# Performance work log

Hardware: AMD Instinct MI355X
Metric: run time of the kernel (lower is better)

Reference implementation:

```python
import jax, jax.numpy as jnp
import numpy as np

N = 100000   # nodes in batch
E = 1600000  # edges
H = 128      # hidden_channels
G = 500      # number of subgraphs (batch ids)
MAXZ = 1000  # max_z
L = 3        # num_layers


def setup_inputs() -> dict:
    key = jax.random.key(0)
    ks = jax.random.split(key, 12)
    s = 1.0 / np.sqrt(H)
    z = jax.random.randint(ks[0], (N,), 0, MAXZ)
    edge_index = jax.random.randint(ks[1], (2, E), 0, N)
    batch = jnp.repeat(jnp.arange(G), N // G)  # sorted graph ids, 200 nodes/graph
    edge_weight = jax.random.uniform(ks[2], (E,), jnp.float32)
    z_table = jax.random.normal(ks[3], (MAXZ, H), jnp.float32) * s
    conv_Ws = tuple(jax.random.normal(ks[4 + i], (H, H), jnp.float32) * s for i in range(L))
    conv_bs = tuple(jnp.zeros((H,), jnp.float32) for _ in range(L))
    lin1_W = jax.random.normal(ks[8], (H, H), jnp.float32) * s
    lin1_b = jnp.zeros((H,), jnp.float32)
    lin2_W = jax.random.normal(ks[9], (H, 1), jnp.float32) * s
    lin2_b = jnp.zeros((1,), jnp.float32)
    return dict(z=z, edge_index=edge_index, batch=batch, edge_weight=edge_weight,
                z_table=z_table, conv_Ws=conv_Ws, conv_bs=conv_bs,
                lin1_W=lin1_W, lin1_b=lin1_b, lin2_W=lin2_W, lin2_b=lin2_b)


def gcn_norm(edge_index, edge_weight, n):
    # add self loops (fill value 1) and symmetric normalization, as in PyG gcn_norm
    loop = jnp.arange(n)
    row = jnp.concatenate([edge_index[0], loop])
    col = jnp.concatenate([edge_index[1], loop])
    w = jnp.concatenate([edge_weight, jnp.ones((n,), edge_weight.dtype)])
    deg = jax.ops.segment_sum(w, col, num_segments=n)
    dinv = jnp.where(deg > 0, jax.lax.rsqrt(deg), 0.0)
    norm = dinv[row] * w * dinv[col]
    return row, col, norm


def gcn_conv(x, row, col, norm, W, b):
    xw = x @ W                                        # [N,H] GEMM first (PyG order)
    msg = norm[:, None] * xw[row]                     # gather + scale  [E+N, H]
    out = jax.ops.segment_sum(msg, col, num_segments=x.shape[0])  # scatter-add
    return out + b


def reference(z, edge_index, batch, edge_weight, z_table, conv_Ws, conv_bs,
              lin1_W, lin1_b, lin2_W, lin2_b):
    x = z_table[z]                                    # z embedding [N,H]
    row, col, norm = gcn_norm(edge_index, edge_weight, x.shape[0])
    for i in range(L - 1):
        x = jax.nn.relu(gcn_conv(x, row, col, norm, conv_Ws[i], conv_bs[i]))
        # dropout is identity in eval mode
    x = gcn_conv(x, row, col, norm, conv_Ws[-1], conv_bs[-1])
    # first occurrence of each graph id in sorted batch == center node indices
    center = jnp.searchsorted(batch, jnp.arange(G))
    h = x[center] * x[center + 1]                     # src * dst center pair
    h = jax.nn.relu(h @ lin1_W + lin1_b)
    return h @ lin2_W + lin2_b                        # [G,1]
```

## Files before the change

### kernel.cpp

```cpp
#include <hip/hip_runtime.h>
#include <hip/hip_bf16.h>

#define H 128
#define CAP 64
#define GBM 64
#define GBN 64
#define BW 128
#define BSH 7
#define BCAP 4096
#define EPB 2048
#define RSHIFT 17
#define RMASK  0x1FFFF

typedef __attribute__((ext_vector_type(8))) short bf16x8;
typedef __attribute__((ext_vector_type(4))) float f32x4;
typedef unsigned long long u64;

__device__ __forceinline__ unsigned short f2b(float f) {
  __hip_bfloat16 h = __float2bfloat16(f);
  union { __hip_bfloat16 h; unsigned short u; } c; c.h = h; return c.u;
}
__device__ __forceinline__ float b2f(unsigned short u) {
  union { unsigned int i; float f; } c; c.i = (unsigned)u << 16; return c.f;
}


__global__ __launch_bounds__(256) void k_binA(const int* __restrict__ row,
    const int* __restrict__ col, const float* __restrict__ ew,
    int* __restrict__ gcur, u64* __restrict__ binned, int E, int NB) {
  __shared__ int hist[1024];
  __shared__ int gbase[1024];
  int tid = threadIdx.x;
  for (int i = tid; i < NB; i += 256) hist[i] = 0;
  __syncthreads();
  int base = blockIdx.x * EPB;
  for (int j = tid; j < EPB; j += 256) {
    int e = base + j;
    if (e < E) atomicAdd(&hist[col[e] >> BSH], 1);
  }
  __syncthreads();
  for (int i = tid; i < NB; i += 256) {
    gbase[i] = atomicAdd(&gcur[i], hist[i]);
    hist[i] = 0;
  }
  __syncthreads();
  for (int j = tid; j < EPB; j += 256) {
    int e = base + j;
    if (e < E) {
      int c = col[e];
      int b = c >> BSH;
      int r = atomicAdd(&hist[b], 1);
      int pos = gbase[b] + r;
      if (pos >= BCAP) pos = BCAP - 1;
      unsigned pk = (unsigned)(c & (BW - 1)) | ((unsigned)row[e] << BSH);
      binned[(size_t)b * BCAP + pos] = (u64)pk | ((u64)(unsigned)__float_as_int(ew[e]) << 32);
    }
  }
}


__global__ __launch_bounds__(256) void k_binB(const int* __restrict__ gcur,
    const u64* __restrict__ binned, int* __restrict__ cnt, float* __restrict__ dinv,
    int2* __restrict__ elist, int n) {
  __shared__ int lcnt[BW];
  __shared__ float lws[BW];
  __shared__ int lcur[BW];
  int b = blockIdx.x, tid = threadIdx.x;
  if (tid < BW) { lcnt[tid] = 0; lws[tid] = 0.f; lcur[tid] = 0; }
  __syncthreads();
  int m = gcur[b];
  if (m > BCAP) m = BCAP;
  const u64* src = binned + (size_t)b * BCAP;
  for (int j = tid; j < m; j += 256) {
    u64 v = src[j];
    int cl = (int)(v & (BW - 1));
    atomicAdd(&lcnt[cl], 1);
    atomicAdd(&lws[cl], __int_as_float((int)(v >> 32)));
  }
  __syncthreads();
  if (tid < BW) {
    int c = b * BW + tid;
    if (c < n) {
      cnt[c] = min(lcnt[tid], CAP);
      dinv[c] = 1.f / sqrtf(1.f + lws[tid]);
    }
  }
  __syncthreads();
  for (int j = tid; j < m; j += 256) {
    u64 v = src[j];
    int cl = (int)(v & (BW - 1));
    int r = atomicAdd(&lcur[cl], 1);
    if (r < CAP) {
      int c = b * BW + cl;
      int rw = (int)((v >> BSH) & RMASK);
      elist[(size_t)c * CAP + r] = make_int2(rw, (int)(v >> 32));
    }
  }
}

__global__ __launch_bounds__(256) void k_pack(const int* __restrict__ cnt,
    int* __restrict__ cntp, const float* __restrict__ dinv, const int* __restrict__ z,
    int2* __restrict__ elist, int n) {
  int wid = (blockIdx.x * 256 + threadIdx.x) >> 4;
  if (wid >= n) return;
  int lane = threadIdx.x & 15;
  int m = min(cnt[wid], CAP);
  int mp = (m + 7) & ~7;
  if (lane == 0) cntp[wid] = mp;
  float dc = dinv[wid];
  for (int j = lane; j < mp; j += 16) {
    size_t idx = (size_t)wid * CAP + j;
    if (j < m) {
      int2 e = elist[idx];
      int r = e.x;
      float nrm = dinv[r] * __int_as_float(e.y) * dc;
      elist[idx] = make_int2(r | (z[r] << RSHIFT), __float_as_int(nrm));
    } else {
      elist[idx] = make_int2(0, 0);
    }
  }
}

__global__ void k_wprep(const float* __restrict__ W, unsigned short* __restrict__ whl) {
  int i = blockIdx.x * 256 + threadIdx.x;
  if (i >= H * H) return;
  int k = i >> 7, n = i & 127;
  float w = W[i];
  unsigned short hi = f2b(w);
  whl[n * H + k] = hi;
  whl[H * H + n * H + k] = f2b(w - b2f(hi));
}


__global__ __launch_bounds__(256) void k_mark(const int* __restrict__ batch, int n,
    int* __restrict__ clist, const int2* __restrict__ elist, const int* __restrict__ cnt,
    unsigned int* __restrict__ bitmap, int nc) {
  int widx = (blockIdx.x * 256 + threadIdx.x) >> 6;
  if (widx >= nc) return;
  int lane = threadIdx.x & 63;
  int g = widx >> 1;
  int lo = 0, hi = n;
  while (lo < hi) { int mid = (lo + hi) >> 1; if (batch[mid] < g) lo = mid + 1; else hi = mid; }
  int v = lo + (widx & 1);
  if (lane == 0) {
    clist[widx] = v;
    atomicOr(&bitmap[v >> 5], 1u << (v & 31));
  }
  int m = min(cnt[v], CAP);
  if (lane < m) {
    int r = elist[(size_t)v * CAP + lane].x & RMASK;
    atomicOr(&bitmap[r >> 5], 1u << (r & 31));
  }
}

__global__ void k_compact(const unsigned int* __restrict__ bitmap,
                          int* __restrict__ slist, int* __restrict__ scount, int n) {
  int i = blockIdx.x * 256 + threadIdx.x;
  if (i >= n) return;
  if (bitmap[i >> 5] & (1u << (i & 31))) slist[atomicAdd(scount, 1)] = i;
}


#define FMA4(A, xs, wv) { A[0] = fmaf(xs, wv.x, A[0]); A[1] = fmaf(xs, wv.y, A[1]); \
                          A[2] = fmaf(xs, wv.z, A[2]); A[3] = fmaf(xs, wv.w, A[3]); }

__global__ __launch_bounds__(256, 2) void k_gemm(const float* __restrict__ X,
    const float* __restrict__ Wg, void* __restrict__ Yv, int Nrows,
    const float* __restrict__ bias, int relu, int outbf) {
  __shared__ float Ws[H][GBN + 4];
  int tid = threadIdx.x;
  int bm = blockIdx.x * GBM;
  int bn = blockIdx.y * GBN;
  for (int i = tid; i < H * (GBN / 4); i += 256) {
    int k = i >> 4, c4 = (i & 15) * 4;
    *(float4*)&Ws[k][c4] = *(const float4*)(Wg + k * H + bn + c4);
  }
  __syncthreads();
  int rg = tid >> 4, cg = tid & 15;
  int cg4 = cg * 4;
  int g0 = bm + rg * 4 + 0, g1 = g0 + 1, g2 = g0 + 2, g3 = g0 + 3;
  const float* xp0; const float* xp1; const float* xp2; const float* xp3;
  {
    int c0 = g0 < Nrows ? g0 : Nrows - 1;
    int c1 = g1 < Nrows ? g1 : Nrows - 1;
    int c2 = g2 < Nrows ? g2 : Nrows - 1;
    int c3 = g3 < Nrows ? g3 : Nrows - 1;
    xp0 = X + (size_t)c0 * H; xp1 = X + (size_t)c1 * H;
    xp2 = X + (size_t)c2 * H; xp3 = X + (size_t)c3 * H;
  }
  float a0[4] = {0,0,0,0}, a1[4] = {0,0,0,0}, a2[4] = {0,0,0,0}, a3[4] = {0,0,0,0};
  #pragma unroll 2
  for (int k = 0; k < H; k += 4) {
    float4 x0 = *(const float4*)(xp0 + k);
    float4 x1 = *(const float4*)(xp1 + k);
    float4 x2 = *(const float4*)(xp2 + k);
    float4 x3 = *(const float4*)(xp3 + k);
    float4 w0 = *(const float4*)&Ws[k + 0][cg4];
    float4 w1 = *(const float4*)&Ws[k + 1][cg4];
    float4 w2 = *(const float4*)&Ws[k + 2][cg4];
    float4 w3 = *(const float4*)&Ws[k + 3][cg4];
    FMA4(a0, x0.x, w0) FMA4(a0, x0.y, w1) FMA4(a0, x0.z, w2) FMA4(a0, x0.w, w3)
    FMA4(a1, x1.x, w0) FMA4(a1, x1.y, w1) FMA4(a1, x1.z, w2) FMA4(a1, x1.w, w3)
    FMA4(a2, x2.x, w0) FMA4(a2, x2.y, w1) FMA4(a2, x2.z, w2) FMA4(a2, x2.w, w3)
    FMA4(a3, x3.x, w0) FMA4(a3, x3.y, w1) FMA4(a3, x3.z, w2) FMA4(a3, x3.w, w3)
  }
  if (bias) {
    float4 bb = *(const float4*)(bias + bn + cg4);
    #pragma unroll
    for (int u = 0; u < 4; ++u) {
      a0[u] += ((const float*)&bb)[u]; a1[u] += ((const float*)&bb)[u];
      a2[u] += ((const float*)&bb)[u]; a3[u] += ((const float*)&bb)[u];
    }
  }
  if (relu) {
    #pragma unroll
    for (int u = 0; u < 4; ++u) {
      a0[u] = fmaxf(a0[u], 0.f); a1[u] = fmaxf(a1[u], 0.f);
      a2[u] = fmaxf(a2[u], 0.f); a3[u] = fmaxf(a3[u], 0.f);
    }
  }
  if (outbf) {
    unsigned short* Yb = (unsigned short*)Yv;
    ushort4 h0 = make_ushort4(f2b(a0[0]), f2b(a0[1]), f2b(a0[2]), f2b(a0[3]));
    ushort4 h1 = make_ushort4(f2b(a1[0]), f2b(a1[1]), f2b(a1[2]), f2b(a1[3]));
    ushort4 h2 = make_ushort4(f2b(a2[0]), f2b(a2[1]), f2b(a2[2]), f2b(a2[3]));
    ushort4 h3 = make_ushort4(f2b(a3[0]), f2b(a3[1]), f2b(a3[2]), f2b(a3[3]));
    if (g0 < Nrows) *(ushort4*)(Yb + (size_t)g0 * H + bn + cg4) = h0;
    if (g1 < Nrows) *(ushort4*)(Yb + (size_t)g1 * H + bn + cg4) = h1;
    if (g2 < Nrows) *(ushort4*)(Yb + (size_t)g2 * H + bn + cg4) = h2;
    if (g3 < Nrows) *(ushort4*)(Yb + (size_t)g3 * H + bn + cg4) = h3;
  } else {
    float* Y = (float*)Yv;
    if (g0 < Nrows) *(float4*)(Y + (size_t)g0 * H + bn + cg4) = make_float4(a0[0], a0[1], a0[2], a0[3]);
    if (g1 < Nrows) *(float4*)(Y + (size_t)g1 * H + bn + cg4) = make_float4(a1[0], a1[1], a1[2], a1[3]);
    if (g2 < Nrows) *(float4*)(Y + (size_t)g2 * H + bn + cg4) = make_float4(a2[0], a2[1], a2[2], a2[3]);
    if (g3 < Nrows) *(float4*)(Y + (size_t)g3 * H + bn + cg4) = make_float4(a3[0], a3[1], a3[2], a3[3]);
  }
}


#define MFMA_GRID 512

__global__ __launch_bounds__(256, 2) void k_gemm_mfma(const unsigned short* __restrict__ Xb,
    const unsigned short* __restrict__ WHL, unsigned short* __restrict__ Yb, int Nrows) {
  __shared__ unsigned short WsH[H * H];
  __shared__ unsigned short WsL[H * H];
  int tid = threadIdx.x;
  {
    const int4* src = (const int4*)WHL;
    int4* dH = (int4*)WsH;
    int4* dL = (int4*)WsL;
    for (int i = tid; i < 2048; i += 256) {
      dH[i] = src[i];
      dL[i] = src[2048 + i];
    }
  }
  __syncthreads();
  int lane = tid & 63, wave = tid >> 6;
  int mrow = lane & 15, h = lane >> 4;
  int ntile = (Nrows + 63) >> 6;
  for (int t = blockIdx.x; t < ntile; t += MFMA_GRID) {
    int Mbase = t * 64 + wave * 16;
    int arow = Mbase + mrow;
    if (arow >= Nrows) arow = Nrows - 1;
    const unsigned short* xr = Xb + (size_t)arow * H;
    bf16x8 a[4];
    #pragma unroll
    for (int kt = 0; kt < 4; ++kt)
      a[kt] = *(const bf16x8*)(xr + kt * 32 + h * 8);
    f32x4 acc[8];
    #pragma unroll
    for (int nt = 0; nt < 8; ++nt) acc[nt] = (f32x4){0.f, 0.f, 0.f, 0.f};
    #pragma unroll
    for (int nt = 0; nt < 8; ++nt) {
      #pragma unroll
      for (int kt = 0; kt < 4; ++kt) {
        int boff = (nt * 16 + mrow) * H + kt * 32 + h * 8;
        bf16x8 bh = *(const bf16x8*)(WsH + boff);
        bf16x8 bl = *(const bf16x8*)(WsL + boff);
        acc[nt] = __builtin_amdgcn_mfma_f32_16x16x32_bf16(a[kt], bh, acc[nt], 0, 0, 0);
        acc[nt] = __builtin_amdgcn_mfma_f32_16x16x32_bf16(a[kt], bl, acc[nt], 0, 0, 0);
      }
    }
    #pragma unroll
    for (int nt = 0; nt < 8; ++nt) {
      int ocol = nt * 16 + mrow;
      #pragma unroll
      for (int r = 0; r < 4; ++r) {
        int orow = Mbase + 4 * h + r;
        if (orow < Nrows) Yb[(size_t)orow * H + ocol] = f2b(acc[nt][r]);
      }
    }
  }
}


__global__ __launch_bounds__(256) void k_aggb_list(const unsigned short* __restrict__ XWB,
    const int2* __restrict__ elist, const int* __restrict__ cntp,
    const float* __restrict__ dinv, const float* __restrict__ bias,
    float* __restrict__ out, const int* __restrict__ slist,
    const int* __restrict__ scount, int relu) {
  int widx = (blockIdx.x * 256 + threadIdx.x) >> 5;
  if (widx >= *scount) return;
  int wid = slist[widx];
  int c4 = threadIdx.x & 31;
  const ushort4* xw4 = (const ushort4*)XWB;
  int m = cntp[wid];
  const int2* ep = elist + (size_t)wid * CAP;
  float dc = dinv[wid];
  float d2 = dc * dc;
  ushort4 s = xw4[(size_t)wid * 32 + c4];
  float4 acc = make_float4(d2 * b2f(s.x), d2 * b2f(s.y), d2 * b2f(s.z), d2 * b2f(s.w));
  for (int j0 = 0; j0 < m; j0 += 8) {
    int2 Ee[8];
    #pragma unroll
    for (int u = 0; u < 8; ++u) Ee[u] = ep[j0 + u];
    ushort4 V[8];
    #pragma unroll
    for (int u = 0; u < 8; ++u) V[u] = xw4[(size_t)(Ee[u].x & RMASK) * 32 + c4];
    #pragma unroll
    for (int u = 0; u < 8; ++u) {
      float nn = __int_as_float(Ee[u].y);
      acc.x = fmaf(nn, b2f(V[u].x), acc.x);
      acc.y = fmaf(nn, b2f(V[u].y), acc.y);
      acc.z = fmaf(nn, b2f(V[u].z), acc.z);
      acc.w = fmaf(nn, b2f(V[u].w), acc.w);
    }
  }
  float4 bb = ((const float4*)bias)[c4];
  acc.x += bb.x; acc.y += bb.y; acc.z += bb.z; acc.w += bb.w;
  if (relu) {
    acc.x = fmaxf(acc.x, 0.f); acc.y = fmaxf(acc.y, 0.f);
    acc.z = fmaxf(acc.z, 0.f); acc.w = fmaxf(acc.w, 0.f);
  }
  ((float4*)out)[(size_t)wid * 32 + c4] = acc;
}


#define EFMA(nn, vv) { acc.x = fmaf(nn, vv.x, acc.x); acc.y = fmaf(nn, vv.y, acc.y); \
                       acc.z = fmaf(nn, vv.z, acc.z); acc.w = fmaf(nn, vv.w, acc.w); }

__global__ __launch_bounds__(256) void k_agg_last(const float* __restrict__ X,
    const int2* __restrict__ elist, const int* __restrict__ cntp,
    const float* __restrict__ dinv, const int* __restrict__ clist,
    float* __restrict__ out, int nc) {
  int widx = (blockIdx.x * 256 + threadIdx.x) >> 5;
  if (widx >= nc) return;
  int v = clist[widx];
  int c4 = threadIdx.x & 31;
  const float4* x4 = (const float4*)X;
  int m = cntp[v];
  const int2* ep = elist + (size_t)v * CAP;
  float dc = dinv[v];
  float d2 = dc * dc;
  float4 s = x4[(size_t)v * 32 + c4];
  float4 acc = make_float4(d2 * s.x, d2 * s.y, d2 * s.z, d2 * s.w);
  for (int j0 = 0; j0 < m; j0 += 8) {
    int2 Ee[8];
    #pragma unroll
    for (int u = 0; u < 8; ++u) Ee[u] = ep[j0 + u];
    float4 V[8];
    #pragma unroll
    for (int u = 0; u < 8; ++u) V[u] = x4[(size_t)(Ee[u].x & RMASK) * 32 + c4];
    #pragma unroll
    for (int u = 0; u < 8; ++u) {
      float nn = __int_as_float(Ee[u].y);
      EFMA(nn, V[u])
    }
  }
  ((float4*)out)[(size_t)widx * 32 + c4] = acc;
}


__global__ __launch_bounds__(256) void k_agg_emb(const unsigned short* __restrict__ ZTW,
    const int* __restrict__ z, const int2* __restrict__ elist, const int* __restrict__ cntp,
    const float* __restrict__ dinv, const float* __restrict__ bias,
    unsigned short* __restrict__ out, int n) {
  int wid = (blockIdx.x * 256 + threadIdx.x) >> 5;
  if (wid >= n) return;
  int c4 = threadIdx.x & 31;
  const ushort4* zt4 = (const ushort4*)ZTW;
  int m = cntp[wid];
  const int2* ep = elist + (size_t)wid * CAP;
  float dc = dinv[wid];
  float d2 = dc * dc;
  ushort4 s = zt4[(size_t)z[wid] * 32 + c4];
  float4 acc = make_float4(d2 * b2f(s.x), d2 * b2f(s.y), d2 * b2f(s.z), d2 * b2f(s.w));
  for (int j0 = 0; j0 < m; j0 += 8) {
    int2 Ee[8];
    #pragma unroll
    for (int u = 0; u < 8; ++u) Ee[u] = ep[j0 + u];
    ushort4 V[8];
    #pragma unroll
    for (int u = 0; u < 8; ++u) V[u] = zt4[(size_t)((unsigned)Ee[u].x >> RSHIFT) * 32 + c4];
    #pragma unroll
    for (int u = 0; u < 8; ++u) {
      float nn = __int_as_float(Ee[u].y);
      acc.x = fmaf(nn, b2f(V[u].x), acc.x);
      acc.y = fmaf(nn, b2f(V[u].y), acc.y);
      acc.z = fmaf(nn, b2f(V[u].z), acc.z);
      acc.w = fmaf(nn, b2f(V[u].w), acc.w);
    }
  }
  float4 bb = ((const float4*)bias)[c4];
  ushort4 o = make_ushort4(f2b(fmaxf(acc.x + bb.x, 0.f)),
                           f2b(fmaxf(acc.y + bb.y, 0.f)),
                           f2b(fmaxf(acc.z + bb.z, 0.f)),
                           f2b(fmaxf(acc.w + bb.w, 0.f)));
  ((ushort4*)out)[(size_t)wid * 32 + c4] = o;
}


__global__ __launch_bounds__(128) void k_head_y(const float* __restrict__ Y,
    const float* __restrict__ W1, const float* __restrict__ b1,
    const float* __restrict__ W2, const float* __restrict__ b2,
    float* __restrict__ out, int G) {
  int g = blockIdx.x, t = threadIdx.x;
  __shared__ float hs[H];
  hs[t] = Y[(size_t)(2 * g) * H + t] * Y[(size_t)(2 * g + 1) * H + t];
  __syncthreads();
  float a = b1[t];
  #pragma unroll 8
  for (int k = 0; k < H; ++k) a = fmaf(hs[k], W1[k * H + t], a);
  a = fmaxf(a, 0.f);
  a *= W2[t];
  for (int off = 32; off > 0; off >>= 1) a += __shfl_down(a, off);
  __shared__ float wsum[2];
  if ((t & 63) == 0) wsum[t >> 6] = a;
  __syncthreads();
  if (t == 0) out[g] = wsum[0] + wsum[1] + b2[0];
}


extern "C" void kernel_launch(void* const* d_in, const int* in_sizes, int n_in,
                              void* d_out, int out_size, void* d_ws, size_t ws_size,
                              hipStream_t stream) {
  const int* z     = (const int*)d_in[0];
  const int* eidx  = (const int*)d_in[1];
  const int* batch = (const int*)d_in[2];
  const float* ew  = (const float*)d_in[3];
  const float* ztab= (const float*)d_in[4];
  const float *W0, *W1, *W2, *b0, *b1, *b2, *l1W, *l1b, *l2W, *l2b;
  if (n_in >= 15) {
    W0 = (const float*)d_in[5];  W1 = (const float*)d_in[6];  W2 = (const float*)d_in[7];
    b0 = (const float*)d_in[8];  b1 = (const float*)d_in[9];  b2 = (const float*)d_in[10];
    l1W = (const float*)d_in[11]; l1b = (const float*)d_in[12];
    l2W = (const float*)d_in[13]; l2b = (const float*)d_in[14];
  } else {
    const float* Wss = (const float*)d_in[5];
    W0 = Wss; W1 = Wss + H * H; W2 = Wss + 2 * H * H;
    const float* bs = (const float*)d_in[6];
    b0 = bs; b1 = bs + H; b2 = bs + 2 * H;
    l1W = (const float*)d_in[7]; l1b = (const float*)d_in[8];
    l2W = (const float*)d_in[9]; l2b = (const float*)d_in[10];
  }
  int N = in_sizes[0];
  int E = in_sizes[3];
  int ZTOT = in_sizes[4];
  int MAXZ = ZTOT / H;
  int G = out_size;
  float* fout = (float*)d_out;
  int NC = 2 * G;
  int MAXS = NC * (CAP + 1);
  int NB = (N + BW - 1) >> BSH;

  size_t woff = 0;
  auto alloc = [&](size_t bytes) {
    void* p = (char*)d_ws + woff;
    woff += (bytes + 255) & ~(size_t)255;
    return p;
  };
  unsigned short* h1b   = (unsigned short*)alloc((size_t)N * H * 2);
  unsigned short* xwb   = (unsigned short*)alloc((size_t)N * H * 2);
  float*          bufB  = (float*)alloc((size_t)N * H * 4);
  unsigned int*   bitmap= (unsigned int*)alloc(((size_t)N + 31) / 32 * 4);
  int*            scount= (int*)alloc(4);
  int*            gcur  = (int*)alloc((size_t)NB * 4);
  float*          dinv  = (float*)alloc((size_t)N * 4);
  int*            cnt   = (int*)alloc((size_t)N * 4);
  int*            cntp  = (int*)alloc((size_t)N * 4);
  unsigned short* ztw   = (unsigned short*)alloc((size_t)ZTOT * 2);
  unsigned short* whl   = (unsigned short*)alloc((size_t)2 * H * H * 2);
  int*            clist = (int*)alloc((size_t)NC * 4);
  int*            slist = (int*)alloc((size_t)MAXS * 4);
  float*          agg2  = (float*)alloc((size_t)NC * H * 4);
  float*          ybuf  = (float*)alloc((size_t)NC * H * 4);
  u64*            binned= (u64*)alloc((size_t)NB * BCAP * 8);
  int2*           elist = (int2*)alloc((size_t)N * CAP * 8);

  const int* erow = eidx;
  const int* ecol = eidx + E;

  size_t zlen = ((((size_t)N + 31) / 32 * 4 + 255) & ~(size_t)255) + 256
              + (((size_t)NB * 4 + 255) & ~(size_t)255);
  hipMemsetAsync(bitmap, 0, zlen, stream);

  int nb = (N + 255) / 256;
  int qgrid = (N + 15) / 16;
  int hgrid = (N + 7) / 8;

  k_binA<<<(E + EPB - 1) / EPB, 256, 0, stream>>>(erow, ecol, ew, gcur, binned, E, NB);
  k_binB<<<NB, 256, 0, stream>>>(gcur, binned, cnt, dinv, elist, N);
  k_pack<<<qgrid, 256, 0, stream>>>(cnt, cntp, dinv, z, elist, N);
  dim3 zgrid((MAXZ + GBM - 1) / GBM, H / GBN);
  k_gemm<<<zgrid, 256, 0, stream>>>(ztab, W0, ztw, MAXZ, nullptr, 0, 1);
  k_wprep<<<(H * H + 255) / 256, 256, 0, stream>>>(W1, whl);
  k_mark<<<(NC + 3) / 4, 256, 0, stream>>>(batch, N, clist, elist, cnt, bitmap, NC);
  k_compact<<<nb, 256, 0, stream>>>(bitmap, slist, scount, N);

  k_agg_emb<<<hgrid, 256, 0, stream>>>(ztw, z, elist, cntp, dinv, b0, h1b, N);
  k_gemm_mfma<<<MFMA_GRID, 256, 0, stream>>>(h1b, whl, xwb, N);
  k_aggb_list<<<(MAXS + 7) / 8, 256, 0, stream>>>(xwb, elist, cntp, dinv, b1, bufB, slist, scount, 1);
  k_agg_last<<<(NC + 7) / 8, 256, 0, stream>>>(bufB, elist, cntp, dinv, clist, agg2, NC);
  dim3 ygrid((NC + GBM - 1) / GBM, H / GBN);
  k_gemm<<<ygrid, 256, 0, stream>>>(agg2, W2, ybuf, NC, b2, 0, 0);

  k_head_y<<<G, 128, 0, stream>>>(ybuf, l1W, l1b, l2W, l2b, fout, G);
}
```

Measured before the change: 248.4 us.

## Fuse edge normalization into bin scatter and unroll aggregation loops by 16

Splits the bin kernel so degree/dinv is computed first. A new pass then writes the final packed elist entries (row|z, normalized weight) directly, replacing the separate pack kernel that re-read and re-wrote the edge lists. Padding goes to multiples of 16, and the three aggregation kernels now process 16 neighbors per iteration for more memory-level parallelism. The cost is a second read of the binned buffer, more padding work, and higher register pressure in the aggregation kernels.

```diff
diff --git a/kernel.cpp b/kernel.cpp
--- a/kernel.cpp
+++ b/kernel.cpp
@@ -60,13 +60,11 @@
 
 
 __global__ __launch_bounds__(256) void k_binB(const int* __restrict__ gcur,
-    const u64* __restrict__ binned, int* __restrict__ cnt, float* __restrict__ dinv,
-    int2* __restrict__ elist, int n) {
+    const u64* __restrict__ binned, int* __restrict__ cnt, float* __restrict__ dinv, int n) {
   __shared__ int lcnt[BW];
   __shared__ float lws[BW];
-  __shared__ int lcur[BW];
   int b = blockIdx.x, tid = threadIdx.x;
-  if (tid < BW) { lcnt[tid] = 0; lws[tid] = 0.f; lcur[tid] = 0; }
+  if (tid < BW) { lcnt[tid] = 0; lws[tid] = 0.f; }
   __syncthreads();
   int m = gcur[b];
   if (m > BCAP) m = BCAP;
@@ -85,38 +83,47 @@
       dinv[c] = 1.f / sqrtf(1.f + lws[tid]);
     }
   }
-  __syncthreads();
+}
+
+
+__global__ __launch_bounds__(256) void k_binPack(const int* __restrict__ gcur,
+    const u64* __restrict__ binned, int* __restrict__ cntp,
+    const float* __restrict__ dinv, const int* __restrict__ z,
+    int2* __restrict__ elist, int n) {
+  __shared__ int lcur[BW];
+  __shared__ float ldin[BW];
+  int b = blockIdx.x, tid = threadIdx.x;
+  if (tid < BW) {
+    lcur[tid] = 0;
+    int c = b * BW + tid;
+    ldin[tid] = (c < n) ? dinv[c] : 0.f;
+  }
+  __syncthreads();
+  int m = gcur[b];
+  if (m > BCAP) m = BCAP;
+  const u64* src = binned + (size_t)b * BCAP;
   for (int j = tid; j < m; j += 256) {
     u64 v = src[j];
     int cl = (int)(v & (BW - 1));
     int r = atomicAdd(&lcur[cl], 1);
     if (r < CAP) {
+      int rw = (int)((v >> BSH) & RMASK);
+      float w = __int_as_float((int)(v >> 32));
+      float nrm = dinv[rw] * w * ldin[cl];
       int c = b * BW + cl;
-      int rw = (int)((v >> BSH) & RMASK);
-      elist[(size_t)c * CAP + r] = make_int2(rw, (int)(v >> 32));
-    }
-  }
-}
-
-__global__ __launch_bounds__(256) void k_pack(const int* __restrict__ cnt,
-    int* __restrict__ cntp, const float* __restrict__ dinv, const int* __restrict__ z,
-    int2* __restrict__ elist, int n) {
-  int wid = (blockIdx.x * 256 + threadIdx.x) >> 4;
-  if (wid >= n) return;
-  int lane = threadIdx.x & 15;
-  int m = min(cnt[wid], CAP);
-  int mp = (m + 7) & ~7;
-  if (lane == 0) cntp[wid] = mp;
-  float dc = dinv[wid];
-  for (int j = lane; j < mp; j += 16) {
-    size_t idx = (size_t)wid * CAP + j;
-    if (j < m) {
-      int2 e = elist[idx];
-      int r = e.x;
-      float nrm = dinv[r] * __int_as_float(e.y) * dc;
-      elist[idx] = make_int2(r | (z[r] << RSHIFT), __float_as_int(nrm));
-    } else {
-      elist[idx] = make_int2(0, 0);
+      elist[(size_t)c * CAP + r] = make_int2(rw | (z[rw] << RSHIFT), __float_as_int(nrm));
+    }
+  }
+  __syncthreads();
+  if (tid < BW) {
+    int c = b * BW + tid;
+    if (c < n) {
+      int mm = min(lcur[tid], CAP);
+      int mp = (mm + 15) & ~15;
+      if (mp > CAP) mp = CAP;
+      cntp[c] = mp;
+      for (int j = mm; j < mp; ++j)
+        elist[(size_t)c * CAP + j] = make_int2(0, 0);
     }
   }
 }
@@ -311,15 +318,15 @@
   float d2 = dc * dc;
   ushort4 s = xw4[(size_t)wid * 32 + c4];
   float4 acc = make_float4(d2 * b2f(s.x), d2 * b2f(s.y), d2 * b2f(s.z), d2 * b2f(s.w));
-  for (int j0 = 0; j0 < m; j0 += 8) {
-    int2 Ee[8];
-    #pragma unroll
-    for (int u = 0; u < 8; ++u) Ee[u] = ep[j0 + u];
-    ushort4 V[8];
-    #pragma unroll
-    for (int u = 0; u < 8; ++u) V[u] = xw4[(size_t)(Ee[u].x & RMASK) * 32 + c4];
-    #pragma unroll
-    for (int u = 0; u < 8; ++u) {
+  for (int j0 = 0; j0 < m; j0 += 16) {
+    int2 Ee[16];
+    #pragma unroll
+    for (int u = 0; u < 16; ++u) Ee[u] = ep[j0 + u];
+    ushort4 V[16];
+    #pragma unroll
+    for (int u = 0; u < 16; ++u) V[u] = xw4[(size_t)(Ee[u].x & RMASK) * 32 + c4];
+    #pragma unroll
+    for (int u = 0; u < 16; ++u) {
       float nn = __int_as_float(Ee[u].y);
       acc.x = fmaf(nn, b2f(V[u].x), acc.x);
       acc.y = fmaf(nn, b2f(V[u].y), acc.y);
@@ -355,15 +362,15 @@
   float d2 = dc * dc;
   float4 s = x4[(size_t)v * 32 + c4];
   float4 acc = make_float4(d2 * s.x, d2 * s.y, d2 * s.z, d2 * s.w);
-  for (int j0 = 0; j0 < m; j0 += 8) {
-    int2 Ee[8];
-    #pragma unroll
-    for (int u = 0; u < 8; ++u) Ee[u] = ep[j0 + u];
-    float4 V[8];
-    #pragma unroll
-    for (int u = 0; u < 8; ++u) V[u] = x4[(size_t)(Ee[u].x & RMASK) * 32 + c4];
-    #pragma unroll
-    for (int u = 0; u < 8; ++u) {
+  for (int j0 = 0; j0 < m; j0 += 16) {
+    int2 Ee[16];
+    #pragma unroll
+    for (int u = 0; u < 16; ++u) Ee[u] = ep[j0 + u];
+    float4 V[16];
+    #pragma unroll
+    for (int u = 0; u < 16; ++u) V[u] = x4[(size_t)(Ee[u].x & RMASK) * 32 + c4];
+    #pragma unroll
+    for (int u = 0; u < 16; ++u) {
       float nn = __int_as_float(Ee[u].y);
       EFMA(nn, V[u])
     }
@@ -386,15 +393,15 @@
   float d2 = dc * dc;
   ushort4 s = zt4[(size_t)z[wid] * 32 + c4];
   float4 acc = make_float4(d2 * b2f(s.x), d2 * b2f(s.y), d2 * b2f(s.z), d2 * b2f(s.w));
-  for (int j0 = 0; j0 < m; j0 += 8) {
-    int2 Ee[8];
-    #pragma unroll
-    for (int u = 0; u < 8; ++u) Ee[u] = ep[j0 + u];
-    ushort4 V[8];
-    #pragma unroll
-    for (int u = 0; u < 8; ++u) V[u] = zt4[(size_t)((unsigned)Ee[u].x >> RSHIFT) * 32 + c4];
-    #pragma unroll
-    for (int u = 0; u < 8; ++u) {
+  for (int j0 = 0; j0 < m; j0 += 16) {
+    int2 Ee[16];
+    #pragma unroll
+    for (int u = 0; u < 16; ++u) Ee[u] = ep[j0 + u];
+    ushort4 V[16];
+    #pragma unroll
+    for (int u = 0; u < 16; ++u) V[u] = zt4[(size_t)((unsigned)Ee[u].x >> RSHIFT) * 32 + c4];
+    #pragma unroll
+    for (int u = 0; u < 16; ++u) {
       float nn = __int_as_float(Ee[u].y);
       acc.x = fmaf(nn, b2f(V[u].x), acc.x);
       acc.y = fmaf(nn, b2f(V[u].y), acc.y);
@@ -496,12 +503,11 @@
   hipMemsetAsync(bitmap, 0, zlen, stream);
 
   int nb = (N + 255) / 256;
-  int qgrid = (N + 15) / 16;
   int hgrid = (N + 7) / 8;
 
   k_binA<<<(E + EPB - 1) / EPB, 256, 0, stream>>>(erow, ecol, ew, gcur, binned, E, NB);
-  k_binB<<<NB, 256, 0, stream>>>(gcur, binned, cnt, dinv, elist, N);
-  k_pack<<<qgrid, 256, 0, stream>>>(cnt, cntp, dinv, z, elist, N);
+  k_binB<<<NB, 256, 0, stream>>>(gcur, binned, cnt, dinv, N);
+  k_binPack<<<NB, 256, 0, stream>>>(gcur, binned, cntp, dinv, z, elist, N);
   dim3 zgrid((MAXZ + GBM - 1) / GBM, H / GBN);
   k_gemm<<<zgrid, 256, 0, stream>>>(ztab, W0, ztw, MAXZ, nullptr, 0, 1);
   k_wprep<<<(H * H + 255) / 256, 256, 0, stream>>>(W1, whl);
```

Result: slower. 263.2 us (+6.0%).
